# Kernel optimization log

Hardware: AMD Instinct MI355X
Metric: run time of the kernel (lower is better)

## Reference

```python
import jax, jax.numpy as jnp
import numpy as np

B, T, IN, H, HH, OUT = 512, 512, 6, 64, 128, 8


def setup_inputs() -> dict:
    key = jax.random.key(0)
    ks = jax.random.split(key, 14)
    def lin(k, fan_in, shape):
        s = 1.0 / np.sqrt(fan_in)
        return jax.random.uniform(k, shape, jnp.float32, -s, s)
    return {
        "x": jax.random.normal(ks[0], (B, T, IN), jnp.float32),
        # initial_linear: input_dim -> hidden
        "W_init": lin(ks[1], IN, (IN, H)), "b_init": lin(ks[2], IN, (H,)),
        # vector-field MLP: hidden -> hh -> hh -> hh -> hidden*input
        "W_in": lin(ks[3], H, (H, HH)),  "b_in": lin(ks[4], H, (HH,)),
        "W_h1": lin(ks[5], HH, (HH, HH)), "b_h1": lin(ks[6], HH, (HH,)),
        "W_h2": lin(ks[7], HH, (HH, HH)), "b_h2": lin(ks[8], HH, (HH,)),
        "W_out": lin(ks[9], HH, (HH, H * IN)), "b_out": lin(ks[10], HH, (H * IN,)),
        # final linear: hidden -> output
        "W_fin": lin(ks[11], H, (H, OUT)), "b_fin": lin(ks[12], H, (OUT,)),
    }


def reference(x, W_init, b_init, W_in, b_in, W_h1, b_h1, W_h2, b_h2,
              W_out, b_out, W_fin, b_fin):
    # vector field: f(h) -> (B, H, IN) matrix; dh/dt = f(h) @ dX/dt
    def vf(h, dX):
        z = jax.nn.relu(h @ W_in + b_in)
        z = jax.nn.relu(z @ W_h1 + b_h1)
        z = jax.nn.relu(z @ W_h2 + b_h2)
        A = jnp.tanh(z @ W_out + b_out).reshape(h.shape[0], H, IN)
        return jnp.einsum("bhi,bi->bh", A, dX)

    # h0 from initial value of the path (spline.evaluate(0) == x[:, 0])
    h0 = x[:, 0] @ W_init + b_init  # (B, H)

    # linear interpolation: dX/dt constant on each unit interval
    dX = jnp.swapaxes(x[:, 1:] - x[:, :-1], 0, 1)  # (T-1, B, IN)

    def rk4_step(h, d):
        k1 = vf(h, d)
        k2 = vf(h + 0.5 * k1, d)
        k3 = vf(h + 0.5 * k2, d)
        k4 = vf(h + k3, d)
        h_new = h + (k1 + 2.0 * k2 + 2.0 * k3 + k4) / 6.0
        return h_new, h_new

    _, hs = jax.lax.scan(rk4_step, h0, dX)  # (T-1, B, H)
    hidden = jnp.concatenate([h0[None], hs], axis=0)  # (T, B, H)
    hidden = jnp.swapaxes(hidden, 0, 1)  # (B, T, H)

    # return_sequences=True -> final linear on all steps
    return hidden @ W_fin + b_fin  # (B, T, OUT)
```

## Files before the change

kernel.cpp:

```cpp
#include <hip/hip_runtime.h>
#include <stdint.h>

namespace {

constexpr int B_   = 512;
constexpr int T_   = 512;
constexpr int IN_  = 6;
constexpr int H_   = 64;
constexpr int HH_  = 128;
constexpr int OUT_ = 8;
constexpr int ME   = 16;

typedef _Float16 f16x8 __attribute__((ext_vector_type(8)));
typedef float    f32x4 __attribute__((ext_vector_type(4)));

__device__ __forceinline__ f32x4 mfma16(f16x8 a, f16x8 b, f32x4 c) {
    return __builtin_amdgcn_mfma_f32_16x16x32_f16(a, b, c, 0, 0, 0);
}

__device__ __forceinline__ f16x8 loadB(const float* __restrict__ W, int N,
                                       int k0, int n0, int lane) {
    f16x8 r;
    const int kb = k0 + ((lane >> 4) << 3);
    const int n  = n0 + (lane & 15);
    #pragma unroll
    for (int s = 0; s < 8; ++s) r[s] = (_Float16)W[(kb + s) * N + n];
    return r;
}

__device__ __forceinline__ f16x8 loadA(const uint32_t* __restrict__ buf, int ks, int lane) {
    uint4 q = *reinterpret_cast<const uint4*>(
        buf + (((ks >> 3) + (lane >> 4)) << 6) + ((lane & 15) << 2));
    return __builtin_bit_cast(f16x8, q);
}

__device__ __forceinline__ uint32_t packh2(float a, float b) {
    union { _Float16 h[2]; uint32_t u; } p;
    p.h[0] = (_Float16)a;
    p.h[1] = (_Float16)b;
    return p.u;
}

__device__ __forceinline__ float tanh_fast(float v) {
    float ax = fabsf(v);
    float e  = __expf(2.0f * ax);
    float r  = 1.0f - 2.0f / (e + 1.0f);
    return copysignf(r, v);
}

__global__ __launch_bounds__(512, 2) void cde_kernel(
    const float* __restrict__ x,
    const float* __restrict__ W_init, const float* __restrict__ b_init,
    const float* __restrict__ W_in,   const float* __restrict__ b_in,
    const float* __restrict__ W_h1,   const float* __restrict__ b_h1,
    const float* __restrict__ W_h2,   const float* __restrict__ b_h2,
    const float* __restrict__ W_out,  const float* __restrict__ b_out,
    const float* __restrict__ W_fin,  const float* __restrict__ b_fin,
    float* __restrict__ out)
{
    const int t    = threadIdx.x;
    const int lane = t & 63;
    const int w    = t >> 6;
    const int le   = lane & 15;
    const int lq2  = lane >> 4;
    const int b0   = blockIdx.x * ME;

    __shared__ alignas(16) uint32_t bufA[16 * 64];
    __shared__ alignas(16) uint32_t bufB[16 * 64];
    __shared__ alignas(16) uint32_t b3s[4 * 512 * 4];
    __shared__ float ppw[8][16 * 49];
    __shared__ float dxs[2][ME * IN_];

    f16x8 b1[2], b2[4], b4[12];
    #pragma unroll
    for (int ks = 0; ks < 2; ++ks) b1[ks] = loadB(W_in, HH_, ks * 32, w * 16, lane);
    #pragma unroll
    for (int ks = 0; ks < 4; ++ks) b2[ks] = loadB(W_h1, HH_, ks * 32, w * 16, lane);
    #pragma unroll
    for (int ks = 0; ks < 4; ++ks) {
        f16x8 v = loadB(W_h2, HH_, ks * 32, w * 16, lane);
        *reinterpret_cast<uint4*>(&b3s[(ks * 512 + t) * 4]) = __builtin_bit_cast(uint4, v);
    }
    #pragma unroll
    for (int tt = 0; tt < 3; ++tt)
        #pragma unroll
        for (int ks = 0; ks < 4; ++ks)
            b4[tt * 4 + ks] = loadB(W_out, 384, ks * 32, w * 48 + tt * 16, lane);

    const float binw = b_in[w * 16 + le];
    const float bh1w = b_h1[w * 16 + le];
    const float bh2w = b_h2[w * 16 + le];
    float bow[3];
    int   imod[3];
    #pragma unroll
    for (int tt = 0; tt < 3; ++tt) {
        int n = w * 48 + tt * 16 + le;
        bow[tt]  = b_out[n];
        imod[tt] = n % 6;
    }

    f16x8 wf0, wf1;
    float bfin_r = 0.f;
    #pragma unroll
    for (int s = 0; s < 8; ++s) { wf0[s] = (_Float16)0.f; wf1[s] = (_Float16)0.f; }
    if (w == 0) {
        #pragma unroll
        for (int s = 0; s < 8; ++s) {
            wf0[s] = (le < 8) ? (_Float16)W_fin[(lq2 * 8 + s) * OUT_ + le] : (_Float16)0.f;
            wf1[s] = (le < 8) ? (_Float16)W_fin[(32 + lq2 * 8 + s) * OUT_ + le] : (_Float16)0.f;
        }
        bfin_r = (le < 8) ? b_fin[le] : 0.f;
    }

    float  xa = 0.f, xb = 0.f;
    size_t xdb = 0;
    if (t < 96) {
        int e = t / 6, i = t - 6 * (t / 6);
        xdb = ((size_t)(b0 + e) * T_) * IN_ + i;
        xa = x[xdb];
        xb = x[xdb + IN_];
        dxs[0][t] = xb - xa;
        xa = xb;
        xb = x[xdb + 2 * IN_];
    }

    float h_reg[2], hacc[2] = {0.f, 0.f};
    {
        const float* xe = x + (size_t)(b0 + le) * T_ * IN_;
        float xr[IN_];
        #pragma unroll
        for (int i = 0; i < IN_; ++i) xr[i] = xe[i];
        #pragma unroll
        for (int p = 0; p < 2; ++p) {
            int r = 8 * w + 2 * lq2 + p;
            float s = b_init[r];
            #pragma unroll
            for (int i = 0; i < IN_; ++i) s += xr[i] * W_init[i * H_ + r];
            h_reg[p] = s;
        }
        *reinterpret_cast<uint32_t*>((_Float16*)bufA + (w * 128 + le * 8 + 2 * lq2)) =
            packh2(h_reg[0], h_reg[1]);
    }
    __syncthreads();

#define OUT_MFMA(TT)                                                           \
    {                                                                          \
        f32x4 oc = {0.f, 0.f, 0.f, 0.f};                                       \
        oc = mfma16(loadA(bufA, 0, lane),  wf0, oc);                           \
        oc = mfma16(loadA(bufA, 32, lane), wf1, oc);                           \
        if (le < 8) {                                                          \
            _Pragma("unroll")                                                  \
            for (int j = 0; j < 4; ++j) {                                      \
                int m = lq2 * 4 + j;                                           \
                out[((size_t)(b0 + m) * T_ + (TT)) * OUT_ + le] = oc[j] + bfin_r; \
            }                                                                  \
        }                                                                      \
    }

    for (int step = 0; step < T_ - 1; ++step) {
        const float* dxc = dxs[step & 1];
        float*       dxn = dxs[(step + 1) & 1];
        #pragma unroll
        for (int s4 = 0; s4 < 4; ++s4) {
            if (s4 == 0 && w == 0) { OUT_MFMA(step) }
            {
                f32x4 acc = {0.f, 0.f, 0.f, 0.f};
                acc = mfma16(loadA(bufA, 0, lane),  b1[0], acc);
                acc = mfma16(loadA(bufA, 32, lane), b1[1], acc);
                int n  = w * 16 + le;
                int bi = (n >> 3) * 128 + (n & 7) + lq2 * 32;
                _Float16* zb = (_Float16*)bufB;
                #pragma unroll
                for (int j = 0; j < 4; ++j)
                    zb[bi + j * 8] = (_Float16)fmaxf(acc[j] + binw, 0.f);
            }
            __syncthreads();

            {
                f32x4 a0 = {0.f, 0.f, 0.f, 0.f};
                f32x4 a1 = {0.f, 0.f, 0.f, 0.f};
                a0 = mfma16(loadA(bufB, 0, lane),  b2[0], a0);
                a1 = mfma16(loadA(bufB, 32, lane), b2[1], a1);
                a0 = mfma16(loadA(bufB, 64, lane), b2[2], a0);
                a1 = mfma16(loadA(bufB, 96, lane), b2[3], a1);
                int n  = w * 16 + le;
                int bi = (n >> 3) * 128 + (n & 7) + lq2 * 32;
                _Float16* zb = (_Float16*)bufA;
                #pragma unroll
                for (int j = 0; j < 4; ++j)
                    zb[bi + j * 8] = (_Float16)fmaxf(a0[j] + a1[j] + bh1w, 0.f);
            }
            __syncthreads();

            {
                f32x4 a0 = {0.f, 0.f, 0.f, 0.f};
                f32x4 a1 = {0.f, 0.f, 0.f, 0.f};
                #pragma unroll
                for (int ks = 0; ks < 4; ++ks) {
                    f16x8 bb = __builtin_bit_cast(f16x8,
                        *reinterpret_cast<const uint4*>(&b3s[(ks * 512 + t) * 4]));
                    if (ks & 1) a1 = mfma16(loadA(bufA, ks * 32, lane), bb, a1);
                    else        a0 = mfma16(loadA(bufA, ks * 32, lane), bb, a0);
                }
                int n  = w * 16 + le;
                int bi = (n >> 3) * 128 + (n & 7) + lq2 * 32;
                _Float16* zb = (_Float16*)bufB;
                #pragma unroll
                for (int j = 0; j < 4; ++j)
                    zb[bi + j * 8] = (_Float16)fmaxf(a0[j] + a1[j] + bh2w, 0.f);
            }
            __syncthreads();

            {
                f32x4 a0 = {0.f, 0.f, 0.f, 0.f};
                f32x4 a1 = {0.f, 0.f, 0.f, 0.f};
                f32x4 a2 = {0.f, 0.f, 0.f, 0.f};
                #pragma unroll
                for (int ks = 0; ks < 4; ++ks) {
                    f16x8 av = loadA(bufB, ks * 32, lane);
                    a0 = mfma16(av, b4[ks],     a0);
                    a1 = mfma16(av, b4[4 + ks], a1);
                    a2 = mfma16(av, b4[8 + ks], a2);
                }
                float* pw = ppw[w];
                #pragma unroll
                for (int j = 0; j < 4; ++j) {
                    int m = lq2 * 4 + j;
                    pw[m * 49 + 0 * 16 + le] = tanh_fast(a0[j] + bow[0]) * dxc[m * 6 + imod[0]];
                    pw[m * 49 + 1 * 16 + le] = tanh_fast(a1[j] + bow[1]) * dxc[m * 6 + imod[1]];
                    pw[m * 49 + 2 * 16 + le] = tanh_fast(a2[j] + bow[2]) * dxc[m * 6 + imod[2]];
                }
                #pragma unroll
                for (int p = 0; p < 2; ++p) {
                    int q = 2 * lq2 + p;
                    const float* pr = &pw[le * 49 + q * 6];
                    float kv = (pr[0] + pr[1]) + (pr[2] + pr[3]) + (pr[4] + pr[5]);
                    hacc[p] += ((s4 == 1 || s4 == 2) ? 2.0f : 1.0f) * kv;
                    if (s4 < 3) {
                        kv = h_reg[p] + ((s4 == 2) ? 1.0f : 0.5f) * kv;
                    } else {
                        h_reg[p] += hacc[p] * (1.0f / 6.0f);
                        hacc[p] = 0.f;
                        kv = h_reg[p];
                    }
                    if (p == 0) a0[0] = kv; else a0[1] = kv;
                }
                *reinterpret_cast<uint32_t*>((_Float16*)bufA + (w * 128 + le * 8 + 2 * lq2)) =
                    packh2(a0[0], a0[1]);
                if (s4 == 3 && t < 96) {
                    dxn[t] = xb - xa;
                    xa = xb;
                    if (step + 3 < T_) xb = x[xdb + (size_t)(step + 3) * IN_];
                }
            }
            __syncthreads();
        }
    }

    if (w == 0) { OUT_MFMA(T_ - 1) }
#undef OUT_MFMA
}

}

extern "C" void kernel_launch(void* const* d_in, const int* in_sizes, int n_in,
                              void* d_out, int out_size, void* d_ws, size_t ws_size,
                              hipStream_t stream) {
    const float* x      = (const float*)d_in[0];
    const float* W_init = (const float*)d_in[1];
    const float* b_init = (const float*)d_in[2];
    const float* W_in   = (const float*)d_in[3];
    const float* b_in   = (const float*)d_in[4];
    const float* W_h1   = (const float*)d_in[5];
    const float* b_h1   = (const float*)d_in[6];
    const float* W_h2   = (const float*)d_in[7];
    const float* b_h2   = (const float*)d_in[8];
    const float* W_out  = (const float*)d_in[9];
    const float* b_out  = (const float*)d_in[10];
    const float* W_fin  = (const float*)d_in[11];
    const float* b_fin  = (const float*)d_in[12];
    float* out = (float*)d_out;

    cde_kernel<<<dim3(B_ / ME), dim3(512), 0, stream>>>(
        x, W_init, b_init, W_in, b_in, W_h1, b_h1, W_h2, b_h2,
        W_out, b_out, W_fin, b_fin, out);
}
```

Baseline: 3.819 ms.

## Halve block to four waves, each computing two output tiles per layer

```diff
diff --git a/kernel.cpp b/kernel.cpp
--- a/kernel.cpp
+++ b/kernel.cpp
@@ -10,6 +10,7 @@
 constexpr int HH_  = 128;
 constexpr int OUT_ = 8;
 constexpr int ME   = 16;
+constexpr int PPR  = 103;
 
 typedef _Float16 f16x8 __attribute__((ext_vector_type(8)));
 typedef float    f32x4 __attribute__((ext_vector_type(4)));
@@ -48,7 +49,7 @@
     return copysignf(r, v);
 }
 
-__global__ __launch_bounds__(512, 2) void cde_kernel(
+__global__ __launch_bounds__(256, 1) void cde_kernel(
     const float* __restrict__ x,
     const float* __restrict__ W_init, const float* __restrict__ b_init,
     const float* __restrict__ W_in,   const float* __restrict__ b_in,
@@ -62,42 +63,42 @@
     const int lane = t & 63;
     const int w    = t >> 6;
     const int le   = lane & 15;
-    const int lq2  = lane >> 4;
+    const int g    = lane >> 4;
     const int b0   = blockIdx.x * ME;
 
     __shared__ alignas(16) uint32_t bufA[16 * 64];
     __shared__ alignas(16) uint32_t bufB[16 * 64];
-    __shared__ alignas(16) uint32_t b3s[4 * 512 * 4];
-    __shared__ float ppw[8][16 * 49];
+    __shared__ float pw[4][16 * PPR];
     __shared__ float dxs[2][ME * IN_];
 
-    f16x8 b1[2], b2[4], b4[12];
-    #pragma unroll
-    for (int ks = 0; ks < 2; ++ks) b1[ks] = loadB(W_in, HH_, ks * 32, w * 16, lane);
-    #pragma unroll
-    for (int ks = 0; ks < 4; ++ks) b2[ks] = loadB(W_h1, HH_, ks * 32, w * 16, lane);
-    #pragma unroll
-    for (int ks = 0; ks < 4; ++ks) {
-        f16x8 v = loadB(W_h2, HH_, ks * 32, w * 16, lane);
-        *reinterpret_cast<uint4*>(&b3s[(ks * 512 + t) * 4]) = __builtin_bit_cast(uint4, v);
-    }
-    #pragma unroll
-    for (int tt = 0; tt < 3; ++tt)
+    f16x8 b1[4], b2[8], b3[8], b4[24];
+    #pragma unroll
+    for (int tt = 0; tt < 2; ++tt)
+        #pragma unroll
+        for (int ks = 0; ks < 2; ++ks)
+            b1[tt * 2 + ks] = loadB(W_in, HH_, ks * 32, 32 * w + 16 * tt, lane);
+    #pragma unroll
+    for (int tt = 0; tt < 2; ++tt)
+        #pragma unroll
+        for (int ks = 0; ks < 4; ++ks) {
+            b2[tt * 4 + ks] = loadB(W_h1, HH_, ks * 32, 32 * w + 16 * tt, lane);
+            b3[tt * 4 + ks] = loadB(W_h2, HH_, ks * 32, 32 * w + 16 * tt, lane);
+        }
+    #pragma unroll
+    for (int tt = 0; tt < 6; ++tt)
         #pragma unroll
         for (int ks = 0; ks < 4; ++ks)
-            b4[tt * 4 + ks] = loadB(W_out, 384, ks * 32, w * 48 + tt * 16, lane);
-
-    const float binw = b_in[w * 16 + le];
-    const float bh1w = b_h1[w * 16 + le];
-    const float bh2w = b_h2[w * 16 + le];
-    float bow[3];
-    int   imod[3];
-    #pragma unroll
-    for (int tt = 0; tt < 3; ++tt) {
-        int n = w * 48 + tt * 16 + le;
-        bow[tt]  = b_out[n];
-        imod[tt] = n % 6;
-    }
+            b4[tt * 4 + ks] = loadB(W_out, 384, ks * 32, 96 * w + 16 * tt, lane);
+
+    float binw[2], bh1w[2], bh2w[2], bow[6];
+    #pragma unroll
+    for (int tt = 0; tt < 2; ++tt) {
+        binw[tt] = b_in[32 * w + 16 * tt + le];
+        bh1w[tt] = b_h1[32 * w + 16 * tt + le];
+        bh2w[tt] = b_h2[32 * w + 16 * tt + le];
+    }
+    #pragma unroll
+    for (int tt = 0; tt < 6; ++tt) bow[tt] = b_out[96 * w + 16 * tt + le];
 
     f16x8 wf0, wf1;
     float bfin_r = 0.f;
@@ -106,8 +107,8 @@
     if (w == 0) {
         #pragma unroll
         for (int s = 0; s < 8; ++s) {
-            wf0[s] = (le < 8) ? (_Float16)W_fin[(lq2 * 8 + s) * OUT_ + le] : (_Float16)0.f;
-            wf1[s] = (le < 8) ? (_Float16)W_fin[(32 + lq2 * 8 + s) * OUT_ + le] : (_Float16)0.f;
+            wf0[s] = (le < 8) ? (_Float16)W_fin[(g * 8 + s) * OUT_ + le] : (_Float16)0.f;
+            wf1[s] = (le < 8) ? (_Float16)W_fin[(32 + g * 8 + s) * OUT_ + le] : (_Float16)0.f;
         }
         bfin_r = (le < 8) ? b_fin[le] : 0.f;
     }
@@ -124,22 +125,23 @@
         xb = x[xdb + 2 * IN_];
     }
 
-    float h_reg[2], hacc[2] = {0.f, 0.f};
+    float h_reg[4], hacc[4] = {0.f, 0.f, 0.f, 0.f};
     {
         const float* xe = x + (size_t)(b0 + le) * T_ * IN_;
         float xr[IN_];
         #pragma unroll
         for (int i = 0; i < IN_; ++i) xr[i] = xe[i];
         #pragma unroll
-        for (int p = 0; p < 2; ++p) {
-            int r = 8 * w + 2 * lq2 + p;
+        for (int p = 0; p < 4; ++p) {
+            int r = 16 * w + 4 * g + p;
             float s = b_init[r];
             #pragma unroll
             for (int i = 0; i < IN_; ++i) s += xr[i] * W_init[i * H_ + r];
             h_reg[p] = s;
         }
-        *reinterpret_cast<uint32_t*>((_Float16*)bufA + (w * 128 + le * 8 + 2 * lq2)) =
-            packh2(h_reg[0], h_reg[1]);
+        const int chunk = 2 * w + (g >> 1);
+        bufA[chunk * 64 + le * 4 + ((2 * g) & 3)]     = packh2(h_reg[0], h_reg[1]);
+        bufA[chunk * 64 + le * 4 + ((2 * g + 1) & 3)] = packh2(h_reg[2], h_reg[3]);
     }
     __syncthreads();
 
@@ -151,102 +153,124 @@
         if (le < 8) {                                                          \
             _Pragma("unroll")                                                  \
             for (int j = 0; j < 4; ++j) {                                      \
-                int m = lq2 * 4 + j;                                           \
+                int m = g * 4 + j;                                             \
                 out[((size_t)(b0 + m) * T_ + (TT)) * OUT_ + le] = oc[j] + bfin_r; \
             }                                                                  \
         }                                                                      \
     }
 
+    float dxr[IN_];
+
     for (int step = 0; step < T_ - 1; ++step) {
         const float* dxc = dxs[step & 1];
         float*       dxn = dxs[(step + 1) & 1];
         #pragma unroll
         for (int s4 = 0; s4 < 4; ++s4) {
-            if (s4 == 0 && w == 0) { OUT_MFMA(step) }
+            if (s4 == 0) {
+                #pragma unroll
+                for (int i = 0; i < IN_; ++i) dxr[i] = dxc[le * 6 + i];
+                if (w == 0) { OUT_MFMA(step) }
+            }
             {
-                f32x4 acc = {0.f, 0.f, 0.f, 0.f};
-                acc = mfma16(loadA(bufA, 0, lane),  b1[0], acc);
-                acc = mfma16(loadA(bufA, 32, lane), b1[1], acc);
-                int n  = w * 16 + le;
-                int bi = (n >> 3) * 128 + (n & 7) + lq2 * 32;
+                f16x8 ha0 = loadA(bufA, 0, lane);
+                f16x8 ha1 = loadA(bufA, 32, lane);
+                f32x4 c0 = {0.f, 0.f, 0.f, 0.f};
+                f32x4 c1 = {0.f, 0.f, 0.f, 0.f};
+                c0 = mfma16(ha0, b1[0], c0); c0 = mfma16(ha1, b1[1], c0);
+                c1 = mfma16(ha0, b1[2], c1); c1 = mfma16(ha1, b1[3], c1);
                 _Float16* zb = (_Float16*)bufB;
                 #pragma unroll
-                for (int j = 0; j < 4; ++j)
-                    zb[bi + j * 8] = (_Float16)fmaxf(acc[j] + binw, 0.f);
+                for (int tt = 0; tt < 2; ++tt) {
+                    int n = 32 * w + 16 * tt + le;
+                    int base = (n >> 3) * 128 + (n & 7);
+                    #pragma unroll
+                    for (int j = 0; j < 4; ++j) {
+                        float v = (tt ? c1[j] : c0[j]) + binw[tt];
+                        zb[base + (4 * g + j) * 8] = (_Float16)fmaxf(v, 0.f);
+                    }
+                }
             }
             __syncthreads();
 
             {
-                f32x4 a0 = {0.f, 0.f, 0.f, 0.f};
-                f32x4 a1 = {0.f, 0.f, 0.f, 0.f};
-                a0 = mfma16(loadA(bufB, 0, lane),  b2[0], a0);
-                a1 = mfma16(loadA(bufB, 32, lane), b2[1], a1);
-                a0 = mfma16(loadA(bufB, 64, lane), b2[2], a0);
-                a1 = mfma16(loadA(bufB, 96, lane), b2[3], a1);
-                int n  = w * 16 + le;
-                int bi = (n >> 3) * 128 + (n & 7) + lq2 * 32;
+                f16x8 a0 = loadA(bufB, 0, lane);
+                f16x8 a1 = loadA(bufB, 32, lane);
+                f16x8 a2 = loadA(bufB, 64, lane);
+                f16x8 a3 = loadA(bufB, 96, lane);
                 _Float16* zb = (_Float16*)bufA;
                 #pragma unroll
-                for (int j = 0; j < 4; ++j)
-                    zb[bi + j * 8] = (_Float16)fmaxf(a0[j] + a1[j] + bh1w, 0.f);
+                for (int tt = 0; tt < 2; ++tt) {
+                    f32x4 u = {0.f, 0.f, 0.f, 0.f};
+                    f32x4 v = {0.f, 0.f, 0.f, 0.f};
+                    u = mfma16(a0, b2[tt * 4 + 0], u); v = mfma16(a1, b2[tt * 4 + 1], v);
+                    u = mfma16(a2, b2[tt * 4 + 2], u); v = mfma16(a3, b2[tt * 4 + 3], v);
+                    int n = 32 * w + 16 * tt + le;
+                    int base = (n >> 3) * 128 + (n & 7);
+                    #pragma unroll
+                    for (int j = 0; j < 4; ++j)
+                        zb[base + (4 * g + j) * 8] = (_Float16)fmaxf(u[j] + v[j] + bh1w[tt], 0.f);
+                }
             }
             __syncthreads();
 
             {
-                f32x4 a0 = {0.f, 0.f, 0.f, 0.f};
-                f32x4 a1 = {0.f, 0.f, 0.f, 0.f};
-                #pragma unroll
-                for (int ks = 0; ks < 4; ++ks) {
-                    f16x8 bb = __builtin_bit_cast(f16x8,
-                        *reinterpret_cast<const uint4*>(&b3s[(ks * 512 + t) * 4]));
-                    if (ks & 1) a1 = mfma16(loadA(bufA, ks * 32, lane), bb, a1);
-                    else        a0 = mfma16(loadA(bufA, ks * 32, lane), bb, a0);
-                }
-                int n  = w * 16 + le;
-                int bi = (n >> 3) * 128 + (n & 7) + lq2 * 32;
+                f16x8 a0 = loadA(bufA, 0, lane);
+                f16x8 a1 = loadA(bufA, 32, lane);
+                f16x8 a2 = loadA(bufA, 64, lane);
+                f16x8 a3 = loadA(bufA, 96, lane);
                 _Float16* zb = (_Float16*)bufB;
                 #pragma unroll
-                for (int j = 0; j < 4; ++j)
-                    zb[bi + j * 8] = (_Float16)fmaxf(a0[j] + a1[j] + bh2w, 0.f);
+                for (int tt = 0; tt < 2; ++tt) {
+                    f32x4 u = {0.f, 0.f, 0.f, 0.f};
+                    f32x4 v = {0.f, 0.f, 0.f, 0.f};
+                    u = mfma16(a0, b3[tt * 4 + 0], u); v = mfma16(a1, b3[tt * 4 + 1], v);
+                    u = mfma16(a2, b3[tt * 4 + 2], u); v = mfma16(a3, b3[tt * 4 + 3], v);
+                    int n = 32 * w + 16 * tt + le;
+                    int base = (n >> 3) * 128 + (n & 7);
+                    #pragma unroll
+                    for (int j = 0; j < 4; ++j)
+                        zb[base + (4 * g + j) * 8] = (_Float16)fmaxf(u[j] + v[j] + bh2w[tt], 0.f);
+                }
             }
             __syncthreads();
 
             {
-                f32x4 a0 = {0.f, 0.f, 0.f, 0.f};
-                f32x4 a1 = {0.f, 0.f, 0.f, 0.f};
-                f32x4 a2 = {0.f, 0.f, 0.f, 0.f};
-                #pragma unroll
-                for (int ks = 0; ks < 4; ++ks) {
-                    f16x8 av = loadA(bufB, ks * 32, lane);
-                    a0 = mfma16(av, b4[ks],     a0);
-                    a1 = mfma16(av, b4[4 + ks], a1);
-                    a2 = mfma16(av, b4[8 + ks], a2);
-                }
-                float* pw = ppw[w];
-                #pragma unroll
-                for (int j = 0; j < 4; ++j) {
-                    int m = lq2 * 4 + j;
-                    pw[m * 49 + 0 * 16 + le] = tanh_fast(a0[j] + bow[0]) * dxc[m * 6 + imod[0]];
-                    pw[m * 49 + 1 * 16 + le] = tanh_fast(a1[j] + bow[1]) * dxc[m * 6 + imod[1]];
-                    pw[m * 49 + 2 * 16 + le] = tanh_fast(a2[j] + bow[2]) * dxc[m * 6 + imod[2]];
-                }
-                #pragma unroll
-                for (int p = 0; p < 2; ++p) {
-                    int q = 2 * lq2 + p;
-                    const float* pr = &pw[le * 49 + q * 6];
-                    float kv = (pr[0] + pr[1]) + (pr[2] + pr[3]) + (pr[4] + pr[5]);
+                f16x8 v0 = loadA(bufB, 0, lane);
+                f16x8 v1 = loadA(bufB, 32, lane);
+                f16x8 v2 = loadA(bufB, 64, lane);
+                f16x8 v3 = loadA(bufB, 96, lane);
+                float* pwl = pw[w];
+                #pragma unroll
+                for (int tt = 0; tt < 6; ++tt) {
+                    f32x4 u  = {0.f, 0.f, 0.f, 0.f};
+                    f32x4 vv = {0.f, 0.f, 0.f, 0.f};
+                    u  = mfma16(v0, b4[tt * 4 + 0], u);
+                    vv = mfma16(v1, b4[tt * 4 + 1], vv);
+                    u  = mfma16(v2, b4[tt * 4 + 2], u);
+                    vv = mfma16(v3, b4[tt * 4 + 3], vv);
+                    #pragma unroll
+                    for (int j = 0; j < 4; ++j)
+                        pwl[(4 * g + j) * PPR + 16 * tt + le] =
+                            tanh_fast(u[j] + vv[j] + bow[tt]);
+                }
+                float hs[4];
+                #pragma unroll
+                for (int p = 0; p < 4; ++p) {
+                    const float* pr = &pwl[le * PPR + (4 * g + p) * 6];
+                    float kv = pr[0] * dxr[0] + pr[1] * dxr[1] + pr[2] * dxr[2]
+                             + pr[3] * dxr[3] + pr[4] * dxr[4] + pr[5] * dxr[5];
                     hacc[p] += ((s4 == 1 || s4 == 2) ? 2.0f : 1.0f) * kv;
                     if (s4 < 3) {
-                        kv = h_reg[p] + ((s4 == 2) ? 1.0f : 0.5f) * kv;
+                        hs[p] = h_reg[p] + ((s4 == 2) ? 1.0f : 0.5f) * kv;
                     } else {
                         h_reg[p] += hacc[p] * (1.0f / 6.0f);
                         hacc[p] = 0.f;
-                        kv = h_reg[p];
+                        hs[p] = h_reg[p];
                     }
-                    if (p == 0) a0[0] = kv; else a0[1] = kv;
-                }
-                *reinterpret_cast<uint32_t*>((_Float16*)bufA + (w * 128 + le * 8 + 2 * lq2)) =
-                    packh2(a0[0], a0[1]);
+                }
+                const int chunk = 2 * w + (g >> 1);
+                bufA[chunk * 64 + le * 4 + ((2 * g) & 3)]     = packh2(hs[0], hs[1]);
+                bufA[chunk * 64 + le * 4 + ((2 * g + 1) & 3)] = packh2(hs[2], hs[3]);
                 if (s4 == 3 && t < 96) {
                     dxn[t] = xb - xa;
                     xa = xb;
@@ -281,7 +305,7 @@
     const float* b_fin  = (const float*)d_in[12];
     float* out = (float*)d_out;
 
-    cde_kernel<<<dim3(B_ / ME), dim3(512), 0, stream>>>(
+    cde_kernel<<<dim3(B_ / ME), dim3(256), 0, stream>>>(
         x, W_init, b_init, W_in, b_in, W_h1, b_h1, W_h2, b_h2,
         W_out, b_out, W_fin, b_fin, out);
 }
```

Measured after the change: 4.884 ms. 1.28x slower.
